# Kernel optimization log

Hardware: AMD Instinct MI355X
Metric: run time of the kernel (lower is better)

Reference implementation:

```python
import jax, jax.numpy as jnp
import numpy as np

B, C = 8192, 10000

def setup_inputs() -> dict:
    key = jax.random.key(0)
    k1, k2, k3 = jax.random.split(key, 3)
    x = jax.random.normal(k1, (B, C), dtype=jnp.float32)
    target = jax.random.randint(k2, (B,), 0, C)
    # soft-label matrix: rows are probability distributions (as produced by update())
    matrix = jax.nn.softmax(jax.random.normal(k3, (C, C), dtype=jnp.float32), axis=-1)
    grad_state = jnp.zeros((C, C), dtype=jnp.float32)
    count = jnp.zeros((C, 1), dtype=jnp.float32)
    return {"x": x, "target": target, "matrix": matrix, "grad_state": grad_state, "count": count}

def reference(x, target, matrix, grad_state, count):
    target = target.reshape(-1)
    logprobs = jax.nn.log_softmax(x, axis=-1)          # [B, C]
    softlabel = matrix[target]                          # gather rows: [B, C]
    loss = jnp.mean(jnp.sum(-softlabel * logprobs, axis=-1))  # reduction='mean'
    # training-branch statistics (detached in original)
    p = jax.nn.softmax(jax.lax.stop_gradient(x), axis=-1)
    pred = jnp.argmax(p, axis=-1)
    correct = (pred == target)                          # [B] bool
    # scatter-add correct probs into per-class rows (replaces python Counter loop)
    add = jax.ops.segment_sum(p * correct[:, None].astype(p.dtype), target, num_segments=C)
    cnt = jax.ops.segment_sum(correct.astype(jnp.float32), target, num_segments=C)[:, None]
    new_grad = grad_state + add
    new_count = count + cnt
    return loss, new_grad, new_count
```

## Files before the change

kernel.cpp:

```cpp
#include <hip/hip_runtime.h>

#define CLS 10000
#define BATCH 8192
#define NGRAD 100000000LL

__device__ __forceinline__ void combine_ms(float& m, float& s, float om, float os) {
  float nm = fmaxf(m, om);
  s = s * __expf(m - nm) + os * __expf(om - nm);
  m = nm;
}

__global__ __launch_bounds__(256) void rowstats_kernel(
    const float* __restrict__ x, const int* __restrict__ target,
    const float* __restrict__ matrix, float* __restrict__ row_loss,
    float* __restrict__ row_logZ, int* __restrict__ row_correct)
{
  int b = blockIdx.x;
  int t = target[b];
  const float4* xr = (const float4*)(x + (size_t)b * CLS);
  const float4* mr = (const float4*)(matrix + (size_t)t * CLS);

  float m = -3.4e38f, s = 0.f, dot = 0.f;
  float bestv = -3.4e38f;
  int besti = 0x7fffffff;

  for (int i = threadIdx.x; i < CLS / 4; i += 256) {
    float4 xv = xr[i];
    float4 mv = mr[i];
    dot += xv.x * mv.x;
    dot += xv.y * mv.y;
    dot += xv.z * mv.z;
    dot += xv.w * mv.w;
    float vals[4] = {xv.x, xv.y, xv.z, xv.w};
#pragma unroll
    for (int j = 0; j < 4; ++j) {
      float v = vals[j];
      int idx = 4 * i + j;
      if (v > bestv || (v == bestv && idx < besti)) { bestv = v; besti = idx; }
      float nm = fmaxf(m, v);
      s = s * __expf(m - nm) + __expf(v - nm);
      m = nm;
    }
  }

#pragma unroll
  for (int off = 32; off > 0; off >>= 1) {
    float om = __shfl_down(m, off);
    float os = __shfl_down(s, off);
    float od = __shfl_down(dot, off);
    float ov = __shfl_down(bestv, off);
    int   oi = __shfl_down(besti, off);
    combine_ms(m, s, om, os);
    dot += od;
    if (ov > bestv || (ov == bestv && oi < besti)) { bestv = ov; besti = oi; }
  }

  __shared__ float sm[4], ss[4], sd[4], sv[4];
  __shared__ int si[4];
  int wave = threadIdx.x >> 6;
  if ((threadIdx.x & 63) == 0) {
    sm[wave] = m; ss[wave] = s; sd[wave] = dot; sv[wave] = bestv; si[wave] = besti;
  }
  __syncthreads();
  if (threadIdx.x == 0) {
    for (int w = 1; w < 4; ++w) {
      combine_ms(m, s, sm[w], ss[w]);
      dot += sd[w];
      if (sv[w] > bestv || (sv[w] == bestv && si[w] < besti)) { bestv = sv[w]; besti = si[w]; }
    }
    float logZ = m + __logf(s);
    row_logZ[b] = logZ;
    row_correct[b] = (besti == t) ? 1 : 0;
    row_loss[b] = logZ - dot;
  }
}

__global__ __launch_bounds__(256) void copy_grad_kernel(
    const float* __restrict__ src, float* __restrict__ out)
{
  const long long N4 = (NGRAD - 4) / 4;
  long long k = (long long)blockIdx.x * blockDim.x + threadIdx.x;
  if (k == 0) {
    out[1] = src[0]; out[2] = src[1]; out[3] = src[2];
    out[NGRAD] = src[NGRAD - 1];
  }
  if (k < N4) {
    const float* s = src + 3 + 4 * k;
    float4 v;
    v.x = s[0]; v.y = s[1]; v.z = s[2]; v.w = s[3];
    ((float4*)(out + 4))[k] = v;
  }
}

__global__ __launch_bounds__(256) void finalize_kernel(
    const float* __restrict__ row_loss, const float* __restrict__ count,
    float* __restrict__ out_loss, float* __restrict__ out_count)
{
  float acc = 0.f;
  for (int i = threadIdx.x; i < BATCH; i += 256) acc += row_loss[i];
#pragma unroll
  for (int off = 32; off > 0; off >>= 1) acc += __shfl_down(acc, off);
  __shared__ float sw[4];
  if ((threadIdx.x & 63) == 0) sw[threadIdx.x >> 6] = acc;
  __syncthreads();
  if (threadIdx.x == 0)
    out_loss[0] = (sw[0] + sw[1] + sw[2] + sw[3]) * (1.0f / BATCH);
  for (int c = threadIdx.x; c < CLS; c += 256) out_count[c] = count[c];
}

__global__ __launch_bounds__(256) void scatter_kernel(
    const float* __restrict__ x, const int* __restrict__ target,
    const float* __restrict__ row_logZ, const int* __restrict__ row_correct,
    float* __restrict__ out_grad, float* __restrict__ out_count)
{
  int b = blockIdx.x;
  if (!row_correct[b]) return;
  int t = target[b];
  float lz = row_logZ[b];
  const float* xr = x + (size_t)b * CLS;
  float* gr = out_grad + (size_t)t * CLS;
  for (int c = threadIdx.x; c < CLS; c += 256)
    atomicAdd(&gr[c], __expf(xr[c] - lz));
  if (threadIdx.x == 0) atomicAdd(&out_count[t], 1.0f);
}

extern "C" void kernel_launch(void* const* d_in, const int* in_sizes, int n_in,
                              void* d_out, int out_size, void* d_ws, size_t ws_size,
                              hipStream_t stream)
{
  const float* x          = (const float*)d_in[0];
  const int*   target     = (const int*)d_in[1];
  const float* matrix     = (const float*)d_in[2];
  const float* grad_state = (const float*)d_in[3];
  const float* count      = (const float*)d_in[4];

  float* out       = (float*)d_out;
  float* out_loss  = out;
  float* out_grad  = out + 1;
  float* out_count = out + 1 + NGRAD;

  float* row_loss    = (float*)d_ws;
  float* row_logZ    = row_loss + BATCH;
  int*   row_correct = (int*)(row_logZ + BATCH);

  rowstats_kernel<<<BATCH, 256, 0, stream>>>(x, target, matrix, row_loss,
                                             row_logZ, row_correct);
  const long long N4 = (NGRAD - 4) / 4;
  int copy_blocks = (int)((N4 + 255) / 256);
  copy_grad_kernel<<<copy_blocks, 256, 0, stream>>>(grad_state, out);
  finalize_kernel<<<1, 256, 0, stream>>>(row_loss, count, out_loss, out_count);
  scatter_kernel<<<BATCH, 256, 0, stream>>>(x, target, row_logZ, row_correct,
                                            out_grad, out_count);
}
```

Measured before the change: 1.060 ms.

## Fuse row stats with grad copy and loss finalize into two kernels

Merges the row-statistics kernel and the large grad_state copy into one grid, using block-index ranges to split the work, and folds the loss reduction into the scatter kernel. This cuts four launches to two and lets the compute-heavy row work overlap with the bandwidth-bound copy. The copy now handles four vectors per thread and uses nontemporal loads and stores, and the x reads in the row pass are also nontemporal. The risk is that nontemporal hints on x lower L2 reuse when the scatter pass reads x again.

Result: no change. 1.049 ms (-1.1%).

```diff
diff --git a/kernel.cpp b/kernel.cpp
--- a/kernel.cpp
+++ b/kernel.cpp
@@ -3,6 +3,14 @@
 #define CLS 10000
 #define BATCH 8192
 #define NGRAD 100000000LL
+
+typedef float v4f __attribute__((ext_vector_type(4)));
+
+#define ROW_BLOCKS BATCH
+#define N4 ((NGRAD - 4) / 4)
+#define COPY_PER_THREAD 4
+#define COPY_CHUNK (256 * COPY_PER_THREAD)
+#define COPY_BLOCKS ((int)((N4 + COPY_CHUNK - 1) / COPY_CHUNK))
 
 __device__ __forceinline__ void combine_ms(float& m, float& s, float om, float os) {
   float nm = fmaxf(m, om);
@@ -10,14 +18,50 @@
   m = nm;
 }
 
-__global__ __launch_bounds__(256) void rowstats_kernel(
+__global__ __launch_bounds__(256) void fused_main(
     const float* __restrict__ x, const int* __restrict__ target,
-    const float* __restrict__ matrix, float* __restrict__ row_loss,
-    float* __restrict__ row_logZ, int* __restrict__ row_correct)
+    const float* __restrict__ matrix, const float* __restrict__ grad_state,
+    const float* __restrict__ count, float* __restrict__ out,
+    float* __restrict__ row_loss, float* __restrict__ row_logZ,
+    int* __restrict__ row_correct)
 {
-  int b = blockIdx.x;
+  int blk = blockIdx.x;
+
+  if (blk == ROW_BLOCKS) {
+    float* out_count = out + 1 + NGRAD;
+    for (int c = threadIdx.x; c < CLS; c += 256) out_count[c] = count[c];
+    if (threadIdx.x == 0) {
+      out[1] = grad_state[0];
+      out[2] = grad_state[1];
+      out[3] = grad_state[2];
+      out[NGRAD] = grad_state[NGRAD - 1];
+    }
+    return;
+  }
+
+  if (blk > ROW_BLOCKS) {
+    long long base = (long long)(blk - (ROW_BLOCKS + 1)) * COPY_CHUNK + threadIdx.x;
+    const float* src = grad_state + 3;
+    v4f* dst = (v4f*)(out + 4);
+#pragma unroll
+    for (int j = 0; j < COPY_PER_THREAD; ++j) {
+      long long k = base + (long long)j * 256;
+      if (k < N4) {
+        const float* s = src + 4 * k;
+        v4f v;
+        v[0] = __builtin_nontemporal_load(s + 0);
+        v[1] = __builtin_nontemporal_load(s + 1);
+        v[2] = __builtin_nontemporal_load(s + 2);
+        v[3] = __builtin_nontemporal_load(s + 3);
+        __builtin_nontemporal_store(v, dst + k);
+      }
+    }
+    return;
+  }
+
+  int b = blk;
   int t = target[b];
-  const float4* xr = (const float4*)(x + (size_t)b * CLS);
+  const v4f* xr = (const v4f*)(x + (size_t)b * CLS);
   const float4* mr = (const float4*)(matrix + (size_t)t * CLS);
 
   float m = -3.4e38f, s = 0.f, dot = 0.f;
@@ -25,13 +69,13 @@
   int besti = 0x7fffffff;
 
   for (int i = threadIdx.x; i < CLS / 4; i += 256) {
-    float4 xv = xr[i];
+    v4f xv = __builtin_nontemporal_load(xr + i);
     float4 mv = mr[i];
-    dot += xv.x * mv.x;
-    dot += xv.y * mv.y;
-    dot += xv.z * mv.z;
-    dot += xv.w * mv.w;
-    float vals[4] = {xv.x, xv.y, xv.z, xv.w};
+    dot += xv[0] * mv.x;
+    dot += xv[1] * mv.y;
+    dot += xv[2] * mv.z;
+    dot += xv[3] * mv.w;
+    float vals[4] = {xv[0], xv[1], xv[2], xv[3]};
 #pragma unroll
     for (int j = 0; j < 4; ++j) {
       float v = vals[j];
@@ -75,50 +119,31 @@
   }
 }
 
-__global__ __launch_bounds__(256) void copy_grad_kernel(
-    const float* __restrict__ src, float* __restrict__ out)
-{
-  const long long N4 = (NGRAD - 4) / 4;
-  long long k = (long long)blockIdx.x * blockDim.x + threadIdx.x;
-  if (k == 0) {
-    out[1] = src[0]; out[2] = src[1]; out[3] = src[2];
-    out[NGRAD] = src[NGRAD - 1];
-  }
-  if (k < N4) {
-    const float* s = src + 3 + 4 * k;
-    float4 v;
-    v.x = s[0]; v.y = s[1]; v.z = s[2]; v.w = s[3];
-    ((float4*)(out + 4))[k] = v;
-  }
-}
-
-__global__ __launch_bounds__(256) void finalize_kernel(
-    const float* __restrict__ row_loss, const float* __restrict__ count,
-    float* __restrict__ out_loss, float* __restrict__ out_count)
-{
-  float acc = 0.f;
-  for (int i = threadIdx.x; i < BATCH; i += 256) acc += row_loss[i];
-#pragma unroll
-  for (int off = 32; off > 0; off >>= 1) acc += __shfl_down(acc, off);
-  __shared__ float sw[4];
-  if ((threadIdx.x & 63) == 0) sw[threadIdx.x >> 6] = acc;
-  __syncthreads();
-  if (threadIdx.x == 0)
-    out_loss[0] = (sw[0] + sw[1] + sw[2] + sw[3]) * (1.0f / BATCH);
-  for (int c = threadIdx.x; c < CLS; c += 256) out_count[c] = count[c];
-}
-
-__global__ __launch_bounds__(256) void scatter_kernel(
+__global__ __launch_bounds__(256) void fused_epilogue(
     const float* __restrict__ x, const int* __restrict__ target,
-    const float* __restrict__ row_logZ, const int* __restrict__ row_correct,
-    float* __restrict__ out_grad, float* __restrict__ out_count)
+    const float* __restrict__ row_loss, const float* __restrict__ row_logZ,
+    const int* __restrict__ row_correct, float* __restrict__ out)
 {
   int b = blockIdx.x;
+
+  if (b == 0) {
+    float acc = 0.f;
+    for (int i = threadIdx.x; i < BATCH; i += 256) acc += row_loss[i];
+#pragma unroll
+    for (int off = 32; off > 0; off >>= 1) acc += __shfl_down(acc, off);
+    __shared__ float sw[4];
+    if ((threadIdx.x & 63) == 0) sw[threadIdx.x >> 6] = acc;
+    __syncthreads();
+    if (threadIdx.x == 0)
+      out[0] = (sw[0] + sw[1] + sw[2] + sw[3]) * (1.0f / BATCH);
+  }
+
   if (!row_correct[b]) return;
   int t = target[b];
   float lz = row_logZ[b];
   const float* xr = x + (size_t)b * CLS;
-  float* gr = out_grad + (size_t)t * CLS;
+  float* gr = out + 1 + (size_t)t * CLS;
+  float* out_count = out + 1 + NGRAD;
   for (int c = threadIdx.x; c < CLS; c += 256)
     atomicAdd(&gr[c], __expf(xr[c] - lz));
   if (threadIdx.x == 0) atomicAdd(&out_count[t], 1.0f);
@@ -134,21 +159,15 @@
   const float* grad_state = (const float*)d_in[3];
   const float* count      = (const float*)d_in[4];
 
-  float* out       = (float*)d_out;
-  float* out_loss  = out;
-  float* out_grad  = out + 1;
-  float* out_count = out + 1 + NGRAD;
+  float* out = (float*)d_out;
 
   float* row_loss    = (float*)d_ws;
   float* row_logZ    = row_loss + BATCH;
   int*   row_correct = (int*)(row_logZ + BATCH);
 
-  rowstats_kernel<<<BATCH, 256, 0, stream>>>(x, target, matrix, row_loss,
-                                             row_logZ, row_correct);
-  const long long N4 = (NGRAD - 4) / 4;
-  int copy_blocks = (int)((N4 + 255) / 256);
-  copy_grad_kernel<<<copy_blocks, 256, 0, stream>>>(grad_state, out);
-  finalize_kernel<<<1, 256, 0, stream>>>(row_loss, count, out_loss, out_count);
-  scatter_kernel<<<BATCH, 256, 0, stream>>>(x, target, row_logZ, row_correct,
-                                            out_grad, out_count);
+  int gridA = ROW_BLOCKS + 1 + COPY_BLOCKS;
+  fused_main<<<gridA, 256, 0, stream>>>(x, target, matrix, grad_state, count,
+                                        out, row_loss, row_logZ, row_correct);
+  fused_epilogue<<<BATCH, 256, 0, stream>>>(x, target, row_loss, row_logZ,
+                                            row_correct, out);
 }
```
